# Optimization experiments

Measured on AMD Instinct MI355X. Metric: run time of the kernel, lower is better.

Reference implementation:

```python
import jax, jax.numpy as jnp
import numpy as np


def setup_inputs() -> dict:
    key = jax.random.key(0)
    kq, kk, kv = jax.random.split(key, 3)
    B, H, S, D = 4, 16, 2048, 64
    q = jax.random.normal(kq, (B, H, S, D), dtype=jnp.float32)
    k = jax.random.normal(kk, (B, H, S, D), dtype=jnp.float32)
    v = jax.random.normal(kv, (B, H, S, D), dtype=jnp.float32)
    # BERT-style additive mask (0 = attend, large negative = masked); all-attend here.
    attention_mask = jnp.zeros((B, 1, 1, S), dtype=jnp.float32)
    return {"q": q, "k": k, "v": v, "attention_mask": attention_mask,
            "attention_head_size": D}


def reference(q, k, v, attention_mask, attention_head_size):
    # scores: [B,H,S,S] = Q K^T / sqrt(d)
    scale = 1.0 / jnp.sqrt(jnp.asarray(attention_head_size, dtype=q.dtype))
    scores = jnp.einsum("bhqd,bhkd->bhqk", q, k) * scale
    scores = scores + attention_mask  # additive mask broadcast over [B,1,1,S]
    probs = jax.nn.softmax(scores, axis=-1)
    # dropout is identity in eval mode (original code's dropout call is broken anyway)
    out = jnp.einsum("bhqk,bhkd->bhqd", probs, v)
    return out
```

## Files before the change

### kernel.cpp

```cpp
#include <hip/hip_runtime.h>


typedef __attribute__((ext_vector_type(8))) short short8;
typedef __attribute__((ext_vector_type(4))) float floatx4;

#define S_LEN 2048
#define D_DIM 64
#define NT    32
#define L2E   1.44269504089f
#define MFIX  12.0f

static __device__ __forceinline__ unsigned short f2b(float x) {
  union { float f; unsigned int u; } c; c.f = x;
  return (unsigned short)((c.u + 0x7FFFu + ((c.u >> 16) & 1u)) >> 16);
}
static __device__ __forceinline__ unsigned int rhu(float x) {
  union { float f; unsigned int u; } c; c.f = x;
  return (c.u + 0x8000u) >> 16;
}
static __device__ __forceinline__ void load_lds16(const void* g, void* l) {
  __builtin_amdgcn_global_load_lds(
      (const __attribute__((address_space(1))) unsigned int*)g,
      (__attribute__((address_space(3))) unsigned int*)l, 16, 0, 0);
}

__global__ __launch_bounds__(256) void prep_kernel(
    const float* __restrict__ kin, const float* __restrict__ vin,
    unsigned short* __restrict__ kb, unsigned short* __restrict__ vt) {
  const int tid = threadIdx.x, bx = blockIdx.x;
  if (bx < 8192) {
    const int i = (bx * 256 + tid) * 4;
    const float4 f = *(const float4*)(kin + i);
    uint2 p;
    p.x = (unsigned)f2b(f.x) | ((unsigned)f2b(f.y) << 16);
    p.y = (unsigned)f2b(f.z) | ((unsigned)f2b(f.w) << 16);
    *(uint2*)(kb + i) = p;
  } else {
    const int b2 = bx - 8192;
    const int bh = b2 >> 4;
    const int k0 = (b2 & 15) * 128;
    const int kg = tid & 15;
    const int dg = tid >> 4;
    const float* vp = vin + ((size_t)bh * S_LEN + k0 + kg * 8) * D_DIM + dg * 4;
    float4 f[8];
#pragma unroll
    for (int j = 0; j < 8; ++j) f[j] = *(const float4*)(vp + j * D_DIM);
    const float* ff = (const float*)&f[0];
#pragma unroll
    for (int i = 0; i < 4; ++i) {
      uint4 o;
      o.x = (unsigned)f2b(ff[0 * 4 + i]) | ((unsigned)f2b(ff[1 * 4 + i]) << 16);
      o.y = (unsigned)f2b(ff[2 * 4 + i]) | ((unsigned)f2b(ff[3 * 4 + i]) << 16);
      o.z = (unsigned)f2b(ff[4 * 4 + i]) | ((unsigned)f2b(ff[5 * 4 + i]) << 16);
      o.w = (unsigned)f2b(ff[6 * 4 + i]) | ((unsigned)f2b(ff[7 * 4 + i]) << 16);
      *(uint4*)(vt + ((size_t)bh * D_DIM + dg * 4 + i) * S_LEN + k0 + kg * 8) = o;
    }
  }
}

union SMem {
  struct {
    unsigned short K[2][64 * 64];
    unsigned short V[2][64 * 64];
  } m;
  float Os[64][68];
};

__global__ __launch_bounds__(256, 3) void flash_kernel(
    const float* __restrict__ qin, const unsigned short* __restrict__ kb,
    const unsigned short* __restrict__ vt, const float* __restrict__ mask,
    float* __restrict__ out) {
  __shared__ SMem sm;
  __shared__ float Ls[4][64];

  const int tid = threadIdx.x;
  const int w = tid >> 6, lane = tid & 63, quad = lane >> 4, lm = lane & 15;
  const int bx = blockIdx.x, bh = blockIdx.y, b = bh >> 4;
  const int q0 = bx * 64;
  const int l7 = lm & 7;

  unsigned short* Qs = sm.m.K[1];
  {
    const int row = tid >> 2, r7 = row & 7;
    const float* qp = qin + ((size_t)(bh * S_LEN + q0 + row)) * D_DIM + (tid & 3) * 16;
#pragma unroll
    for (int h = 0; h < 2; ++h) {
      const int chunk = (tid & 3) * 2 + h;
      float4 a = *(const float4*)(qp + h * 8);
      float4 c = *(const float4*)(qp + h * 8 + 4);
      uint4 o;
      o.x = (unsigned)f2b(a.x * 0.125f) | ((unsigned)f2b(a.y * 0.125f) << 16);
      o.y = (unsigned)f2b(a.z * 0.125f) | ((unsigned)f2b(a.w * 0.125f) << 16);
      o.z = (unsigned)f2b(c.x * 0.125f) | ((unsigned)f2b(c.y * 0.125f) << 16);
      o.w = (unsigned)f2b(c.z * 0.125f) | ((unsigned)f2b(c.w * 0.125f) << 16);
      *(uint4*)&Qs[row * 64 + ((chunk ^ r7) * 8)] = o;
    }
  }

  const int rl = lane >> 3, cl = lane & 7;
  const int swz = (cl ^ rl) * 8;
  const unsigned short* kp0 = kb + (size_t)bh * S_LEN * D_DIM + (w * 16 + rl) * 64 + swz;
  const unsigned short* kp1 = kp0 + 8 * 64;
  const unsigned short* vp0 = vt + (size_t)bh * D_DIM * S_LEN + (w * 16 + rl) * S_LEN + swz;
  const unsigned short* vp1 = vp0 + 8 * S_LEN;

  load_lds16(kp0, &sm.m.K[0][(w * 16) * 64]);
  load_lds16(kp1, &sm.m.K[0][(w * 16 + 8) * 64]);
  load_lds16(vp0, &sm.m.V[0][(w * 16) * 64]);
  load_lds16(vp1, &sm.m.V[0][(w * 16 + 8) * 64]);

  const float* mrow = mask + b * S_LEN + w * 16 + quad * 4;
  floatx4 mc;
  {
    const floatx4 ml = *(const floatx4*)mrow;
#pragma unroll
    for (int r = 0; r < 4; ++r) mc[r] = fmaf(ml[r], L2E, -MFIX * L2E);
  }

  __syncthreads();

  short8 bq[4][2];
#pragma unroll
  for (int qs = 0; qs < 4; ++qs) {
    bq[qs][0] = *(const short8*)&Qs[(qs * 16 + lm) * 64 + ((quad ^ l7) * 8)];
    bq[qs][1] = *(const short8*)&Qs[(qs * 16 + lm) * 64 + (((4 + quad) ^ l7) * 8)];
  }
  __syncthreads();

  const int kidx0 = (w * 16 + lm) * 64 + ((quad ^ l7) * 8);
  const int kidx1 = (w * 16 + lm) * 64 + (((4 + quad) ^ l7) * 8);
  const int vc0 = (((2 * w + (quad >> 1)) & 7) ^ l7) * 8 + 4 * (quad & 1);

  floatx4 o[4][4];
#pragma unroll
  for (int dt = 0; dt < 4; ++dt)
#pragma unroll
    for (int qs = 0; qs < 4; ++qs) o[dt][qs] = (floatx4){0.f, 0.f, 0.f, 0.f};
  float lsum[4] = {0.f, 0.f, 0.f, 0.f};

  for (int t = 0; t < NT; ++t) {
    if (t > 0) __syncthreads();
    const int buf = t & 1, nbuf = buf ^ 1;
    if (t + 1 < NT) {
      const size_t off = (size_t)(t + 1) * 4096;
      load_lds16(kp0 + off, &sm.m.K[nbuf][(w * 16) * 64]);
      load_lds16(kp1 + off, &sm.m.K[nbuf][(w * 16 + 8) * 64]);
      load_lds16(vp0 + (t + 1) * 64, &sm.m.V[nbuf][(w * 16) * 64]);
      load_lds16(vp1 + (t + 1) * 64, &sm.m.V[nbuf][(w * 16 + 8) * 64]);
    }
    floatx4 mnext;
    {
      const int tn = (t + 1 < NT) ? (t + 1) : 0;
      mnext = *(const floatx4*)(mrow + tn * 64);
    }

    const unsigned short* Kb = sm.m.K[buf];
    const unsigned short* Vb = sm.m.V[buf];
    const short8 ak0 = *(const short8*)&Kb[kidx0];
    const short8 ak1 = *(const short8*)&Kb[kidx1];

    short8 bp[4];
#pragma unroll
    for (int qs = 0; qs < 4; ++qs) {
      floatx4 st = (floatx4){0.f, 0.f, 0.f, 0.f};
      st = __builtin_amdgcn_mfma_f32_16x16x32_bf16(ak0, bq[qs][0], st, 0, 0, 0);
      st = __builtin_amdgcn_mfma_f32_16x16x32_bf16(ak1, bq[qs][1], st, 0, 0, 0);
      float p[4];
#pragma unroll
      for (int r = 0; r < 4; ++r) {
        p[r] = __builtin_amdgcn_exp2f(fmaf(st[r], L2E, mc[r]));
        lsum[qs] += p[r];
      }
      union { unsigned int u[4]; short8 s; } pb;
      pb.u[0] = rhu(p[0]) | (rhu(p[1]) << 16);
      pb.u[1] = rhu(p[2]) | (rhu(p[3]) << 16);
      pb.u[2] = 0; pb.u[3] = 0;
      bp[qs] = pb.s;
    }

#pragma unroll
    for (int dt = 0; dt < 4; ++dt) {
      union { uint2 u2[2]; short8 s; } av;
      av.u2[0] = *(const uint2*)&Vb[(dt * 16 + lm) * 64 + vc0];
      av.u2[1] = av.u2[0];
#pragma unroll
      for (int qs = 0; qs < 4; ++qs)
        o[dt][qs] = __builtin_amdgcn_mfma_f32_16x16x32_bf16(av.s, bp[qs], o[dt][qs], 0, 0, 0);
    }

#pragma unroll
    for (int r = 0; r < 4; ++r) mc[r] = fmaf(mnext[r], L2E, -MFIX * L2E);
  }

#pragma unroll
  for (int qs = 0; qs < 4; ++qs) {
    float v = lsum[qs];
    v += __shfl_xor(v, 16, 64);
    v += __shfl_xor(v, 32, 64);
    lsum[qs] = v;
  }
  if (quad == 0) {
#pragma unroll
    for (int qs = 0; qs < 4; ++qs) Ls[w][qs * 16 + lm] = lsum[qs];
  }

#pragma unroll
  for (int ph = 0; ph < 4; ++ph) {
    __syncthreads();
    if (w == ph) {
#pragma unroll
      for (int dt = 0; dt < 4; ++dt)
#pragma unroll
        for (int qs = 0; qs < 4; ++qs) {
          float* dst = &sm.Os[qs * 16 + lm][dt * 16 + quad * 4];
          if (ph == 0) {
            *(floatx4*)dst = o[dt][qs];
          } else {
            floatx4 cur = *(const floatx4*)dst;
            *(floatx4*)dst = cur + o[dt][qs];
          }
        }
    }
  }
  __syncthreads();

  {
    const int q = tid >> 2, dc = (tid & 3) * 16;
    const float l = Ls[0][q] + Ls[1][q] + Ls[2][q] + Ls[3][q];
    const float inv = 1.0f / l;
    float* outp = out + ((size_t)(bh * S_LEN + q0 + q)) * D_DIM + dc;
#pragma unroll
    for (int i = 0; i < 4; ++i) {
      floatx4 v = *(const floatx4*)&sm.Os[q][dc + i * 4];
      v *= inv;
      *(floatx4*)(outp + i * 4) = v;
    }
  }
}

extern "C" void kernel_launch(void* const* d_in, const int* in_sizes, int n_in,
                              void* d_out, int out_size, void* d_ws, size_t ws_size,
                              hipStream_t stream) {
  const float* q = (const float*)d_in[0];
  const float* k = (const float*)d_in[1];
  const float* v = (const float*)d_in[2];
  const float* mask = (const float*)d_in[3];
  float* out = (float*)d_out;

  unsigned short* kb = (unsigned short*)d_ws;
  unsigned short* vt = kb + (size_t)64 * S_LEN * D_DIM;

  prep_kernel<<<8192 + 1024, 256, 0, stream>>>(k, v, kb, vt);
  flash_kernel<<<dim3(32, 64), 256, 0, stream>>>(q, kb, vt, mask, out);
}
```

Measured before the change: 268.5 us.

## Pack two key tiles per PV MFMA using triple-buffered V

The PV product previously fed each 16x16x32 MFMA with only half its K dimension filled: the upper half of P was zero and the V fragment was duplicated. It now accumulates P from two consecutive key tiles into the low and high halves and issues the PV MFMAs every other iteration, halving their number. To keep the previous tile's V resident, V moves to a rotating triple buffer, which adds LDS use and may lower occupancy. The loop is unrolled by two.

```diff
diff --git a/kernel.cpp b/kernel.cpp
--- a/kernel.cpp
+++ b/kernel.cpp
@@ -61,7 +61,7 @@
 union SMem {
   struct {
     unsigned short K[2][64 * 64];
-    unsigned short V[2][64 * 64];
+    unsigned short V[3][64 * 64];
   } m;
   float Os[64][68];
 };
@@ -103,11 +103,12 @@
   const unsigned short* kp1 = kp0 + 8 * 64;
   const unsigned short* vp0 = vt + (size_t)bh * D_DIM * S_LEN + (w * 16 + rl) * S_LEN + swz;
   const unsigned short* vp1 = vp0 + 8 * S_LEN;
-
-  load_lds16(kp0, &sm.m.K[0][(w * 16) * 64]);
-  load_lds16(kp1, &sm.m.K[0][(w * 16 + 8) * 64]);
-  load_lds16(vp0, &sm.m.V[0][(w * 16) * 64]);
-  load_lds16(vp1, &sm.m.V[0][(w * 16 + 8) * 64]);
+  const int ldsA = (w * 16) * 64, ldsB = (w * 16 + 8) * 64;
+
+  load_lds16(kp0, &sm.m.K[0][ldsA]);
+  load_lds16(kp1, &sm.m.K[0][ldsB]);
+  load_lds16(vp0, &sm.m.V[0][ldsA]);
+  load_lds16(vp1, &sm.m.V[0][ldsB]);
 
   const float* mrow = mask + b * S_LEN + w * 16 + quad * 4;
   floatx4 mc;
@@ -131,22 +132,29 @@
   const int kidx1 = (w * 16 + lm) * 64 + (((4 + quad) ^ l7) * 8);
   const int vc0 = (((2 * w + (quad >> 1)) & 7) ^ l7) * 8 + 4 * (quad & 1);
 
+  unsigned short* vTm1 = sm.m.V[2];
+  unsigned short* vT   = sm.m.V[0];
+  unsigned short* vTp1 = sm.m.V[1];
+
   floatx4 o[4][4];
 #pragma unroll
   for (int dt = 0; dt < 4; ++dt)
 #pragma unroll
     for (int qs = 0; qs < 4; ++qs) o[dt][qs] = (floatx4){0.f, 0.f, 0.f, 0.f};
   float lsum[4] = {0.f, 0.f, 0.f, 0.f};
-
+  uint4 pb[4];
+
+#pragma unroll 2
   for (int t = 0; t < NT; ++t) {
     if (t > 0) __syncthreads();
-    const int buf = t & 1, nbuf = buf ^ 1;
+    const unsigned short* kcur = (t & 1) ? sm.m.K[1] : sm.m.K[0];
+    unsigned short* knext = (t & 1) ? sm.m.K[0] : sm.m.K[1];
     if (t + 1 < NT) {
       const size_t off = (size_t)(t + 1) * 4096;
-      load_lds16(kp0 + off, &sm.m.K[nbuf][(w * 16) * 64]);
-      load_lds16(kp1 + off, &sm.m.K[nbuf][(w * 16 + 8) * 64]);
-      load_lds16(vp0 + (t + 1) * 64, &sm.m.V[nbuf][(w * 16) * 64]);
-      load_lds16(vp1 + (t + 1) * 64, &sm.m.V[nbuf][(w * 16 + 8) * 64]);
+      load_lds16(kp0 + off, knext + ldsA);
+      load_lds16(kp1 + off, knext + ldsB);
+      load_lds16(vp0 + (t + 1) * 64, vTp1 + ldsA);
+      load_lds16(vp1 + (t + 1) * 64, vTp1 + ldsB);
     }
     floatx4 mnext;
     {
@@ -154,12 +162,9 @@
       mnext = *(const floatx4*)(mrow + tn * 64);
     }
 
-    const unsigned short* Kb = sm.m.K[buf];
-    const unsigned short* Vb = sm.m.V[buf];
-    const short8 ak0 = *(const short8*)&Kb[kidx0];
-    const short8 ak1 = *(const short8*)&Kb[kidx1];
-
-    short8 bp[4];
+    const short8 ak0 = *(const short8*)&kcur[kidx0];
+    const short8 ak1 = *(const short8*)&kcur[kidx1];
+
 #pragma unroll
     for (int qs = 0; qs < 4; ++qs) {
       floatx4 st = (floatx4){0.f, 0.f, 0.f, 0.f};
@@ -171,23 +176,29 @@
         p[r] = __builtin_amdgcn_exp2f(fmaf(st[r], L2E, mc[r]));
         lsum[qs] += p[r];
       }
-      union { unsigned int u[4]; short8 s; } pb;
-      pb.u[0] = rhu(p[0]) | (rhu(p[1]) << 16);
-      pb.u[1] = rhu(p[2]) | (rhu(p[3]) << 16);
-      pb.u[2] = 0; pb.u[3] = 0;
-      bp[qs] = pb.s;
-    }
-
-#pragma unroll
-    for (int dt = 0; dt < 4; ++dt) {
-      union { uint2 u2[2]; short8 s; } av;
-      av.u2[0] = *(const uint2*)&Vb[(dt * 16 + lm) * 64 + vc0];
-      av.u2[1] = av.u2[0];
-#pragma unroll
-      for (int qs = 0; qs < 4; ++qs)
-        o[dt][qs] = __builtin_amdgcn_mfma_f32_16x16x32_bf16(av.s, bp[qs], o[dt][qs], 0, 0, 0);
-    }
-
+      const unsigned lo = rhu(p[0]) | (rhu(p[1]) << 16);
+      const unsigned hi = rhu(p[2]) | (rhu(p[3]) << 16);
+      if ((t & 1) == 0) { pb[qs].x = lo; pb[qs].y = hi; }
+      else             { pb[qs].z = lo; pb[qs].w = hi; }
+    }
+
+    if (t & 1) {
+#pragma unroll
+      for (int dt = 0; dt < 4; ++dt) {
+        const int vrow = (dt * 16 + lm) * 64 + vc0;
+        union { uint2 u2[2]; short8 s; } av;
+        av.u2[0] = *(const uint2*)&vTm1[vrow];
+        av.u2[1] = *(const uint2*)&vT[vrow];
+#pragma unroll
+        for (int qs = 0; qs < 4; ++qs) {
+          union { uint4 u; short8 s; } bp;
+          bp.u = pb[qs];
+          o[dt][qs] = __builtin_amdgcn_mfma_f32_16x16x32_bf16(av.s, bp.s, o[dt][qs], 0, 0, 0);
+        }
+      }
+    }
+
+    unsigned short* tmp = vTm1; vTm1 = vT; vT = vTp1; vTp1 = tmp;
 #pragma unroll
     for (int r = 0; r < 4; ++r) mc[r] = fmaf(mnext[r], L2E, -MFIX * L2E);
   }
```

Measured after the change: 239.3 us. 10.9% less time.
